# Performance work log

Hardware: AMD Instinct MI355X
Metric: run time of the kernel (lower is better)

The kernel has to match this reference:

```python
import jax, jax.numpy as jnp
import numpy as np

DIM = 128
HEADS = 4
DH = 32
SCALE = DH ** -0.5


def _ln(x, g, b):
    m = x.mean(-1, keepdims=True)
    v = x.var(-1, keepdims=True)
    return (x - m) / jnp.sqrt(v + 1e-5) * g + b


def setup_inputs() -> dict:
    key = jax.random.key(0)
    ks = jax.random.split(key, 16)
    B, N, H, W, HK, WK = 2, 6, 48, 48, 24, 24
    d, hd = DIM, HEADS * DH
    p = lambda k, s: (jax.random.normal(k, s, jnp.float32) * 0.02)
    return {
        "q": jax.random.normal(ks[0], (B, N, d, H, W), jnp.float32),
        "k": jax.random.normal(ks[1], (B, N, d, HK, WK), jnp.float32),
        "v": jax.random.normal(ks[2], (B, N, d, HK, WK), jnp.float32),
        "skip": jax.random.normal(ks[3], (B, d, H, W), jnp.float32),
        "lnq_g": jnp.ones(d), "lnq_b": jnp.zeros(d),
        "Wq": p(ks[4], (d, hd)), "bq": jnp.zeros(hd),
        "lnk_g": jnp.ones(d), "lnk_b": jnp.zeros(d),
        "Wk": p(ks[5], (d, hd)), "bk": jnp.zeros(hd),
        "lnv_g": jnp.ones(d), "lnv_b": jnp.zeros(d),
        "Wv": p(ks[6], (d, hd)), "bv": jnp.zeros(hd),
        "Wp": p(ks[7], (hd, d)), "bp": jnp.zeros(d),
        "pre_g": jnp.ones(d), "pre_b": jnp.zeros(d),
        "W1": p(ks[8], (d, 2 * d)), "b1": jnp.zeros(2 * d),
        "W2": p(ks[9], (2 * d, d)), "b2": jnp.zeros(d),
        "post_g": jnp.ones(d), "post_b": jnp.zeros(d),
    }


def reference(q, k, v, skip, lnq_g, lnq_b, Wq, bq, lnk_g, lnk_b, Wk, bk,
              lnv_g, lnv_b, Wv, bv, Wp, bp, pre_g, pre_b, W1, b1, W2, b2,
              post_g, post_b):
    B, N, d, H, W = q.shape
    _, _, _, HK, WK = k.shape
    Q, K = H * W, HK * WK
    # b n d H W -> b n (H W) d
    qx = q.transpose(0, 1, 3, 4, 2).reshape(B, N, Q, d)
    kx = k.transpose(0, 1, 3, 4, 2).reshape(B, N, K, d)
    vx = v.transpose(0, 1, 3, 4, 2).reshape(B, N * K, d)
    # norm + linear projections
    qp = _ln(qx, lnq_g, lnq_b) @ Wq + bq  # (B,N,Q,HEADS*DH)
    kp = _ln(kx, lnk_g, lnk_b) @ Wk + bk
    vp = _ln(vx, lnv_g, lnv_b) @ Wv + bv  # (B,N*K,HEADS*DH)
    # split heads: b ... (m d) -> (b m) ... d
    qp = qp.reshape(B, N, Q, HEADS, DH).transpose(0, 3, 1, 2, 4).reshape(B * HEADS, N, Q, DH)
    kp = kp.reshape(B, N, K, HEADS, DH).transpose(0, 3, 1, 2, 4).reshape(B * HEADS, N, K, DH)
    vp = vp.reshape(B, N * K, HEADS, DH).transpose(0, 2, 1, 3).reshape(B * HEADS, N * K, DH)
    # per-view scores, then softmax jointly over (n K)
    scores = SCALE * jnp.einsum('bnqd,bnkd->bnqk', qp, kp)
    scores = scores.transpose(0, 2, 1, 3).reshape(B * HEADS, Q, N * K)
    a = jax.nn.softmax(scores, axis=-1)
    out = jnp.einsum('bqk,bkd->bqd', a, vp)  # (B*HEADS, Q, DH)
    # merge heads: (b m) Q d -> b Q (m d)
    z = out.reshape(B, HEADS, Q, DH).transpose(0, 2, 1, 3).reshape(B, Q, HEADS * DH)
    z = z @ Wp + bp
    z = z + skip.transpose(0, 2, 3, 1).reshape(B, Q, d)
    z = _ln(z, pre_g, pre_b)
    z = z + (jax.nn.gelu(z @ W1 + b1, approximate=False) @ W2 + b2)
    z = _ln(z, post_g, post_b)
    return z.reshape(B, H, W, d).transpose(0, 3, 1, 2)
```

## Files before the change

kernel.cpp:

```cpp
#include <hip/hip_runtime.h>
#include <cmath>

#define B_    2
#define N_    6
#define D_    128
#define Q_    2304
#define K_    576
#define NK_   3456
#define HEADS_ 4
#define DH_   32
#define SCALE_ 0.17677669529663687f
#define SCLOG2E_ 0.25504672615621814f

typedef __attribute__((ext_vector_type(8))) short bf16x8;
typedef __attribute__((ext_vector_type(4))) float f32x4;

#if defined(__has_builtin)
#if __has_builtin(__builtin_amdgcn_cvt_pk_bf16_f32)
#define HAS_PK_BF16 1
#endif
#endif

static __device__ __forceinline__ unsigned short f2bf(float f) {
  union { float f; unsigned u; } x; x.f = f;
  unsigned u = x.u + 0x7fffu + ((x.u >> 16) & 1u);
  return (unsigned short)(u >> 16);
}
static __device__ __forceinline__ unsigned pkbf(float a, float b) {
#ifdef HAS_PK_BF16
  typedef __attribute__((ext_vector_type(2))) __bf16 vbf2;
  union { vbf2 v; unsigned u; } cv;
  cv.v = __builtin_amdgcn_cvt_pk_bf16_f32(a, b);
  return cv.u;
#else
  return (unsigned)f2bf(a) | ((unsigned)f2bf(b) << 16);
#endif
}

static __device__ __forceinline__ void pl32sw(unsigned &a, unsigned &b) {
  asm("v_permlane32_swap_b32 %0, %1" : "+v"(a), "+v"(b));
}
static __device__ __forceinline__ void pl16sw(unsigned &a, unsigned &b) {
  asm("v_permlane16_swap_b32 %0, %1" : "+v"(a), "+v"(b));
}

__global__ __launch_bounds__(256) void k_prep_wt(
    const float* __restrict__ Wq, const float* __restrict__ Wk,
    const float* __restrict__ Wv, const float* __restrict__ Wp,
    const float* __restrict__ W1, const float* __restrict__ W2,
    unsigned short* __restrict__ WTq, unsigned short* __restrict__ WTk,
    unsigned short* __restrict__ WTv, unsigned short* __restrict__ WTp,
    unsigned short* __restrict__ WT1, unsigned short* __restrict__ WT2)
{
  __shared__ float tile[32][33];
  const int wb = blockIdx.x, t = threadIdx.x;
  const float* src; unsigned short* dst; int Kd, J, tl;
  if      (wb < 16) { src = Wq; dst = WTq; Kd = 128; J = 128; tl = wb; }
  else if (wb < 32) { src = Wk; dst = WTk; Kd = 128; J = 128; tl = wb - 16; }
  else if (wb < 48) { src = Wv; dst = WTv; Kd = 128; J = 128; tl = wb - 32; }
  else if (wb < 64) { src = Wp; dst = WTp; Kd = 128; J = 128; tl = wb - 48; }
  else if (wb < 96) { src = W1; dst = WT1; Kd = 128; J = 256; tl = wb - 64; }
  else              { src = W2; dst = WT2; Kd = 256; J = 128; tl = wb - 96; }
  const int njt = J >> 5;
  const int tj = tl % njt, tk = tl / njt;
#pragma unroll
  for (int i = 0; i < 4; ++i) {
    int idx = t + 256 * i;
    int r = idx >> 5, c = idx & 31;
    tile[r][c] = src[(size_t)(tk * 32 + r) * J + tj * 32 + c];
  }
  __syncthreads();
#pragma unroll
  for (int i = 0; i < 2; ++i) {
    int idx = t + 256 * i;
    int rr = idx >> 4, c2 = (idx & 15) << 1;
    *(unsigned*)&dst[(size_t)(tj * 32 + rr) * Kd + tk * 32 + c2] =
        pkbf(tile[c2][rr], tile[c2 + 1][rr]);
  }
}

__global__ __launch_bounds__(256) void k_ln_proj_all(
    const float* __restrict__ qin, const float* __restrict__ kin,
    const float* __restrict__ vin,
    const float* __restrict__ lnq_g, const float* __restrict__ lnq_b,
    const float* __restrict__ lnk_g, const float* __restrict__ lnk_b,
    const float* __restrict__ lnv_g, const float* __restrict__ lnv_b,
    const unsigned short* __restrict__ WTq, const unsigned short* __restrict__ WTk,
    const unsigned short* __restrict__ WTv,
    const float* __restrict__ bq, const float* __restrict__ bk,
    const float* __restrict__ bv,
    unsigned short* __restrict__ QPh, unsigned short* __restrict__ KPh,
    unsigned short* __restrict__ VPTh)
{
  __shared__ float xs[32][132];
  __shared__ unsigned short xh[32][136];
  __shared__ float gs[128], bs[128];
  __shared__ float mu[32], rsd[32];
  const int t = threadIdx.x;
  const int bid = blockIdx.x;

  const float* x; const unsigned short* WT; const float* g; const float* bl;
  const float* bias; int S, blk, mode; float osc;
  if (bid < 864)       { mode = 0; blk = bid;        x = qin; WT = WTq; g = lnq_g; bl = lnq_b; bias = bq; S = Q_; osc = SCLOG2E_; }
  else if (bid < 1080) { mode = 0; blk = bid - 864;  x = kin; WT = WTk; g = lnk_g; bl = lnk_b; bias = bk; S = K_; osc = 1.0f; }
  else                 { mode = 1; blk = bid - 1080; x = vin; WT = WTv; g = lnv_g; bl = lnv_b; bias = bv; S = K_; osc = 1.0f; }
  const int ntile = S >> 5;
  const int o  = blk / ntile;
  const int s0 = (blk % ntile) << 5;

  if (t < 128) { gs[t] = g[t]; bs[t] = bl[t]; }
  const float* xb = x + (size_t)o * 128 * (size_t)S + s0;
#pragma unroll
  for (int i = 0; i < 4; ++i) {
    int idx = t + 256 * i;
    int c = idx >> 3, s4 = (idx & 7) << 2;
    float4 xv = *(const float4*)&xb[(size_t)c * S + s4];
    xs[s4 + 0][c] = xv.x; xs[s4 + 1][c] = xv.y;
    xs[s4 + 2][c] = xv.z; xs[s4 + 3][c] = xv.w;
  }
  __syncthreads();
  {
    int s = t >> 3, l8 = t & 7;
    float sum = 0.f, sq = 0.f;
    for (int c = l8; c < 128; c += 8) { float v = xs[s][c]; sum += v; sq += v * v; }
#pragma unroll
    for (int off = 4; off > 0; off >>= 1) {
      sum += __shfl_down(sum, off, 8);
      sq  += __shfl_down(sq,  off, 8);
    }
    if (l8 == 0) {
      float mth = sum * 0.0078125f;
      float var = sq * 0.0078125f - mth * mth;
      mu[s] = mth; rsd[s] = rsqrtf(var + 1e-5f);
    }
  }
  __syncthreads();
#pragma unroll
  for (int i = 0; i < 8; ++i) {
    int idx = t + 256 * i;
    int s = idx >> 6, c2 = (idx & 63) << 1;
    float y0 = (xs[s][c2]     - mu[s]) * rsd[s] * gs[c2]     + bs[c2];
    float y1 = (xs[s][c2 + 1] - mu[s]) * rsd[s] * gs[c2 + 1] + bs[c2 + 1];
    *(unsigned*)&xh[s][c2] = pkbf(y0, y1);
  }
  __syncthreads();
  const int w = t >> 6, lane = t & 63, quad = lane >> 4, l16 = lane & 15;
  const f32x4 zf = {0.f, 0.f, 0.f, 0.f};
  f32x4 acc[2][2] = {{zf, zf}, {zf, zf}};
#pragma unroll
  for (int kc = 0; kc < 4; ++kc) {
    bf16x8 a0 = *(const bf16x8*)&xh[l16][kc * 32 + quad * 8];
    bf16x8 a1 = *(const bf16x8*)&xh[16 + l16][kc * 32 + quad * 8];
    bf16x8 b0 = *(const bf16x8*)&WT[(size_t)(w * 32 + l16) * 128 + kc * 32 + quad * 8];
    bf16x8 b1 = *(const bf16x8*)&WT[(size_t)(w * 32 + 16 + l16) * 128 + kc * 32 + quad * 8];
    acc[0][0] = __builtin_amdgcn_mfma_f32_16x16x32_bf16(a0, b0, acc[0][0], 0, 0, 0);
    acc[0][1] = __builtin_amdgcn_mfma_f32_16x16x32_bf16(a0, b1, acc[0][1], 0, 0, 0);
    acc[1][0] = __builtin_amdgcn_mfma_f32_16x16x32_bf16(a1, b0, acc[1][0], 0, 0, 0);
    acc[1][1] = __builtin_amdgcn_mfma_f32_16x16x32_bf16(a1, b1, acc[1][1], 0, 0, 0);
  }
  if (mode == 0) {
    unsigned short* outh = (bid < 864) ? QPh : KPh;
    __syncthreads();
#pragma unroll
    for (int mt = 0; mt < 2; ++mt)
#pragma unroll
      for (int nt = 0; nt < 2; ++nt) {
        int col = w * 32 + nt * 16 + l16;
        float bc = bias[col];
#pragma unroll
        for (int r = 0; r < 4; ++r)
          xh[mt * 16 + quad * 4 + r][col] = f2bf((acc[mt][nt][r] + bc) * osc);
      }
    __syncthreads();
#pragma unroll
    for (int i = 0; i < 2; ++i) {
      int s = i * 16 + (t >> 4), c8 = (t & 15) << 3;
      *(uint4*)&outh[((size_t)o * S + s0 + s) * 128 + c8] = *(uint4*)&xh[s][c8];
    }
  } else {
    const int b = o / 6, n = o % 6;
#pragma unroll
    for (int mt = 0; mt < 2; ++mt)
#pragma unroll
      for (int nt = 0; nt < 2; ++nt) {
        int col = w * 32 + nt * 16 + l16;
        int hh = col >> 5, dh = col & 31;
        float bc = bias[col];
        ushort4 pk;
        *(unsigned*)&pk.x = pkbf(acc[mt][nt][0] + bc, acc[mt][nt][1] + bc);
        *(unsigned*)&pk.z = pkbf(acc[mt][nt][2] + bc, acc[mt][nt][3] + bc);
        int s = n * 576 + s0 + mt * 16 + quad * 4;
        *(ushort4*)&VPTh[((size_t)(b * 4 + hh) * 32 + dh) * (size_t)NK_ + s] = pk;
      }
  }
}

__global__ __launch_bounds__(256) void k_attn_mfma(
    const unsigned short* __restrict__ QPh, const unsigned short* __restrict__ KPh,
    const unsigned short* __restrict__ VPTh, float* __restrict__ PO,
    float* __restrict__ Pl, int sh)
{
  __shared__ float ol[4][16][32];
  __shared__ float ll[4][2][4][16];
  const int t = threadIdx.x;
  const int w = t >> 6, lane = t & 63;
  const int quad = lane >> 4, l16 = lane & 15;
  const int qt = blockIdx.x % 72;
  const int rest = blockIdx.x / 72;
  const int bhx = rest & 7, ks = rest >> 3;
  const int bb = bhx >> 2, h = bhx & 3;
  const int q0 = qt << 5;

  const unsigned short* vbase = VPTh + (size_t)bhx * 32 * (size_t)NK_;
  const f32x4 zf = {0.f, 0.f, 0.f, 0.f};
  f32x4 o00 = zf, o01 = zf, o10 = zf, o11 = zf;
  float lsum0 = 0.f, lsum1 = 0.f;

  const int m8 = ks * 4 + w;
  int c0 = (108 * m8) >> sh, c1 = (108 * (m8 + 1)) >> sh;

  while (c0 < c1) {
    const int nn = c0 / 18;
    const int cend = min(c1, (nn + 1) * 18);
    const unsigned short* kb = &KPh[((size_t)(bb * 6 + nn) * K_) * 128 + h * 32];
    const unsigned short* qb = &QPh[((size_t)(bb * 6 + nn) * Q_ + q0) * 128 + h * 32];
    bf16x8 qc0 = *(const bf16x8*)&qb[(size_t)l16 * 128 + quad * 8];
    bf16x8 qc1 = *(const bf16x8*)&qb[(size_t)(16 + l16) * 128 + quad * 8];

    int kl = (c0 - nn * 18) << 5;
    bf16x8 kf0 = *(const bf16x8*)&kb[(size_t)(kl + l16) * 128 + quad * 8];
    bf16x8 kf1 = *(const bf16x8*)&kb[(size_t)(kl + 16 + l16) * 128 + quad * 8];
    const unsigned short* vb = vbase + ((size_t)c0 << 5);
    bf16x8 pv0 = *(const bf16x8*)&vb[(size_t)l16 * NK_ + quad * 8];
    bf16x8 pv1 = *(const bf16x8*)&vb[(size_t)(16 + l16) * NK_ + quad * 8];
    f32x4 s00 = __builtin_amdgcn_mfma_f32_16x16x32_bf16(kf0, qc0, zf, 0, 0, 0);
    f32x4 s01 = __builtin_amdgcn_mfma_f32_16x16x32_bf16(kf1, qc0, zf, 0, 0, 0);
    f32x4 s10 = __builtin_amdgcn_mfma_f32_16x16x32_bf16(kf0, qc1, zf, 0, 0, 0);
    f32x4 s11 = __builtin_amdgcn_mfma_f32_16x16x32_bf16(kf1, qc1, zf, 0, 0, 0);

    for (int kc = c0; kc < cend; ++kc) {
      const int kln = (kc + 1 - nn * 18) << 5;
      bf16x8 nk0 = *(const bf16x8*)&kb[(size_t)(kln + l16) * 128 + quad * 8];
      bf16x8 nk1 = *(const bf16x8*)&kb[(size_t)(kln + 16 + l16) * 128 + quad * 8];
      const unsigned short* vbn = vbase + ((size_t)(kc + 1) << 5);
      bf16x8 nv0 = *(const bf16x8*)&vbn[(size_t)l16 * NK_ + quad * 8];
      bf16x8 nv1 = *(const bf16x8*)&vbn[(size_t)(16 + l16) * NK_ + quad * 8];

      float a00 = __builtin_amdgcn_exp2f(s00.x), a01 = __builtin_amdgcn_exp2f(s00.y);
      float a02 = __builtin_amdgcn_exp2f(s00.z), a03 = __builtin_amdgcn_exp2f(s00.w);
      float a10 = __builtin_amdgcn_exp2f(s01.x), a11 = __builtin_amdgcn_exp2f(s01.y);
      float a12 = __builtin_amdgcn_exp2f(s01.z), a13 = __builtin_amdgcn_exp2f(s01.w);
      lsum0 += (a00 + a01 + a02 + a03) + (a10 + a11 + a12 + a13);
      float b00 = __builtin_amdgcn_exp2f(s10.x), b01 = __builtin_amdgcn_exp2f(s10.y);
      float b02 = __builtin_amdgcn_exp2f(s10.z), b03 = __builtin_amdgcn_exp2f(s10.w);
      float b10 = __builtin_amdgcn_exp2f(s11.x), b11 = __builtin_amdgcn_exp2f(s11.y);
      float b12 = __builtin_amdgcn_exp2f(s11.z), b13 = __builtin_amdgcn_exp2f(s11.w);
      lsum1 += (b00 + b01 + b02 + b03) + (b10 + b11 + b12 + b13);

      unsigned xA0 = pkbf(a00, a01), xA1 = pkbf(a02, a03);
      unsigned xB0 = pkbf(a10, a11), xB1 = pkbf(a12, a13);
      unsigned yA0 = pkbf(b00, b01), yA1 = pkbf(b02, b03);
      unsigned yB0 = pkbf(b10, b11), yB1 = pkbf(b12, b13);
      pl32sw(xA0, xB0); pl32sw(xA1, xB1);
      pl16sw(xA0, xB0); pl16sw(xA1, xB1);
      pl32sw(yA0, yB0); pl32sw(yA1, yB1);
      pl16sw(yA0, yB0); pl16sw(yA1, yB1);
      union { unsigned u[4]; bf16x8 v; } f0, f1;
      f0.u[0] = xA0; f0.u[1] = xA1; f0.u[2] = xB0; f0.u[3] = xB1;
      f1.u[0] = yA0; f1.u[1] = yA1; f1.u[2] = yB0; f1.u[3] = yB1;

      __builtin_amdgcn_s_setprio(1);
      o00 = __builtin_amdgcn_mfma_f32_16x16x32_bf16(f0.v, pv0, o00, 0, 0, 0);
      o01 = __builtin_amdgcn_mfma_f32_16x16x32_bf16(f0.v, pv1, o01, 0, 0, 0);
      o10 = __builtin_amdgcn_mfma_f32_16x16x32_bf16(f1.v, pv0, o10, 0, 0, 0);
      o11 = __builtin_amdgcn_mfma_f32_16x16x32_bf16(f1.v, pv1, o11, 0, 0, 0);
      s00 = __builtin_amdgcn_mfma_f32_16x16x32_bf16(nk0, qc0, zf, 0, 0, 0);
      s01 = __builtin_amdgcn_mfma_f32_16x16x32_bf16(nk1, qc0, zf, 0, 0, 0);
      s10 = __builtin_amdgcn_mfma_f32_16x16x32_bf16(nk0, qc1, zf, 0, 0, 0);
      s11 = __builtin_amdgcn_mfma_f32_16x16x32_bf16(nk1, qc1, zf, 0, 0, 0);
      __builtin_amdgcn_s_setprio(0);
      pv0 = nv0; pv1 = nv1;
    }
    c0 = cend;
  }

  ll[w][0][quad][l16] = lsum0;
  ll[w][1][quad][l16] = lsum1;
#pragma unroll
  for (int tt = 0; tt < 2; ++tt) {
    __syncthreads();
    f32x4 t0 = tt ? o10 : o00;
    f32x4 t1 = tt ? o11 : o01;
#pragma unroll
    for (int r = 0; r < 4; ++r) {
      ol[w][quad * 4 + r][l16]      = t0[r];
      ol[w][quad * 4 + r][16 + l16] = t1[r];
    }
    __syncthreads();
    const int q = t >> 4, i16 = t & 15, dd = i16 << 1;
    float a0 = 0.f, a1 = 0.f;
#pragma unroll
    for (int ww = 0; ww < 4; ++ww) { a0 += ol[ww][q][dd]; a1 += ol[ww][q][dd + 1]; }
    float2 r2; r2.x = a0; r2.y = a1;
    *(float2*)&PO[(((size_t)ks * 8 + bhx) * Q_ + q0 + tt * 16 + q) * 32 + dd] = r2;
    if (i16 == 0) {
      float l = 0.f;
#pragma unroll
      for (int ww = 0; ww < 4; ++ww)
#pragma unroll
        for (int qq = 0; qq < 4; ++qq) l += ll[ww][tt][qq][q];
      Pl[((size_t)ks * 8 + bhx) * Q_ + q0 + tt * 16 + q] = l;
    }
  }
}

__global__ __launch_bounds__(512) void k_tail(
    const float* __restrict__ PO, const float* __restrict__ Pl,
    const unsigned short* __restrict__ WTp, const float* __restrict__ bp,
    const float* __restrict__ skip,
    const float* __restrict__ pre_g, const float* __restrict__ pre_b,
    const unsigned short* __restrict__ WT1, const float* __restrict__ b1,
    const unsigned short* __restrict__ WT2, const float* __restrict__ b2,
    const float* __restrict__ post_g, const float* __restrict__ post_b,
    float* __restrict__ out, int nks)
{
  __shared__ float xs[16][132];
  __shared__ unsigned short xh[16][136];
  __shared__ unsigned short hb[16][264];
  __shared__ float g1s[128], b1s[128], g2s[128], b2s[128];
  __shared__ float mu[16], rsd[16];
  const int t = threadIdx.x;
  const int row0 = blockIdx.x << 4;
  const int bb = row0 / Q_, hw0 = row0 % Q_;
  const int w = t >> 6, lane = t & 63, quad = lane >> 4, l16 = lane & 15;
  const f32x4 zf = {0.f, 0.f, 0.f, 0.f};

  if (t < 128) { g1s[t] = pre_g[t]; b1s[t] = pre_b[t]; g2s[t] = post_g[t]; b2s[t] = post_b[t]; }
#pragma unroll
  for (int i = 0; i < 2; ++i) {
    int idx = t + 512 * i;
    int s = idx >> 6, c2 = (idx & 63) << 1;
    int q = hw0 + s;
    int h = c2 >> 5, dh = c2 & 31;
    size_t bq = (size_t)(bb * 4 + h) * Q_ + q;
    size_t i0 = bq * 32 + dh;
    float px = 0.f, py = 0.f, l = 0.f;
    for (int p = 0; p < nks; ++p) {
      float2 pp = *(const float2*)&PO[(size_t)p * 589824 + i0];
      px += pp.x; py += pp.y;
      l += Pl[(size_t)p * 18432 + bq];
    }
    float inv = 1.f / l;
    *(unsigned*)&xh[s][c2] = pkbf(px * inv, py * inv);
  }
  __syncthreads();
  {
    f32x4 acc = zf;
    const int col = w * 16 + l16;
#pragma unroll
    for (int kc = 0; kc < 4; ++kc) {
      bf16x8 a0 = *(const bf16x8*)&xh[l16][kc * 32 + quad * 8];
      bf16x8 b0 = *(const bf16x8*)&WTp[(size_t)col * 128 + kc * 32 + quad * 8];
      acc = __builtin_amdgcn_mfma_f32_16x16x32_bf16(a0, b0, acc, 0, 0, 0);
    }
    float bc = bp[col];
    float4 sk = *(const float4*)&skip[((size_t)bb * 128 + col) * Q_ + hw0 + quad * 4];
    xs[quad * 4 + 0][col] = acc[0] + bc + sk.x;
    xs[quad * 4 + 1][col] = acc[1] + bc + sk.y;
    xs[quad * 4 + 2][col] = acc[2] + bc + sk.z;
    xs[quad * 4 + 3][col] = acc[3] + bc + sk.w;
  }
  __syncthreads();
  {
    int s = t >> 5, lg = t & 31;
    float sum = 0.f, sq = 0.f;
    for (int c = lg; c < 128; c += 32) { float v = xs[s][c]; sum += v; sq += v * v; }
#pragma unroll
    for (int off = 16; off > 0; off >>= 1) {
      sum += __shfl_down(sum, off, 32);
      sq  += __shfl_down(sq,  off, 32);
    }
    if (lg == 0) {
      float mth = sum * 0.0078125f;
      float var = sq * 0.0078125f - mth * mth;
      mu[s] = mth; rsd[s] = rsqrtf(var + 1e-5f);
    }
  }
  __syncthreads();
#pragma unroll
  for (int i = 0; i < 2; ++i) {
    int idx = t + 512 * i;
    int s = idx >> 6, c2 = (idx & 63) << 1;
    float y0 = (xs[s][c2]     - mu[s]) * rsd[s] * g1s[c2]     + b1s[c2];
    float y1 = (xs[s][c2 + 1] - mu[s]) * rsd[s] * g1s[c2 + 1] + b1s[c2 + 1];
    xs[s][c2] = y0; xs[s][c2 + 1] = y1;
    *(unsigned*)&xh[s][c2] = pkbf(y0, y1);
  }
  __syncthreads();
  {
#pragma unroll
    for (int nt = 0; nt < 2; ++nt) {
      const int col = w * 32 + nt * 16 + l16;
      f32x4 acc = zf;
#pragma unroll
      for (int kc = 0; kc < 4; ++kc) {
        bf16x8 a0 = *(const bf16x8*)&xh[l16][kc * 32 + quad * 8];
        bf16x8 b0 = *(const bf16x8*)&WT1[(size_t)col * 128 + kc * 32 + quad * 8];
        acc = __builtin_amdgcn_mfma_f32_16x16x32_bf16(a0, b0, acc, 0, 0, 0);
      }
      float bc = b1[col];
#pragma unroll
      for (int r = 0; r < 4; ++r) {
        float hx = acc[r] + bc;
        hb[quad * 4 + r][col] =
            f2bf(0.5f * hx * (1.f + erff(hx * 0.7071067811865476f)));
      }
    }
  }
  __syncthreads();
  {
    f32x4 acc = zf;
    const int col = w * 16 + l16;
#pragma unroll
    for (int kc = 0; kc < 8; ++kc) {
      bf16x8 a0 = *(const bf16x8*)&hb[l16][kc * 32 + quad * 8];
      bf16x8 b0 = *(const bf16x8*)&WT2[(size_t)col * 256 + kc * 32 + quad * 8];
      acc = __builtin_amdgcn_mfma_f32_16x16x32_bf16(a0, b0, acc, 0, 0, 0);
    }
    float bc = b2[col];
#pragma unroll
    for (int r = 0; r < 4; ++r) {
      int row = quad * 4 + r;
      xs[row][col] = acc[r] + bc + xs[row][col];
    }
  }
  __syncthreads();
  {
    int s = t >> 5, lg = t & 31;
    float sum = 0.f, sq = 0.f;
    for (int c = lg; c < 128; c += 32) { float v = xs[s][c]; sum += v; sq += v * v; }
#pragma unroll
    for (int off = 16; off > 0; off >>= 1) {
      sum += __shfl_down(sum, off, 32);
      sq  += __shfl_down(sq,  off, 32);
    }
    if (lg == 0) {
      float mth = sum * 0.0078125f;
      float var = sq * 0.0078125f - mth * mth;
      mu[s] = mth; rsd[s] = rsqrtf(var + 1e-5f);
    }
  }
  __syncthreads();
#pragma unroll
  for (int i = 0; i < 4; ++i) {
    int idx = t + 512 * i;
    int s = idx & 15, c = idx >> 4;
    out[(size_t)bb * (128 * (size_t)Q_) + (size_t)c * Q_ + hw0 + s] =
        (xs[s][c] - mu[s]) * rsd[s] * g2s[c] + b2s[c];
  }
}

extern "C" void kernel_launch(void* const* d_in, const int* in_sizes, int n_in,
                              void* d_out, int out_size, void* d_ws, size_t ws_size,
                              hipStream_t stream) {
  const float* q     = (const float*)d_in[0];
  const float* k     = (const float*)d_in[1];
  const float* v     = (const float*)d_in[2];
  const float* skip  = (const float*)d_in[3];
  const float* lnq_g = (const float*)d_in[4];
  const float* lnq_b = (const float*)d_in[5];
  const float* Wq    = (const float*)d_in[6];
  const float* bq    = (const float*)d_in[7];
  const float* lnk_g = (const float*)d_in[8];
  const float* lnk_b = (const float*)d_in[9];
  const float* Wk    = (const float*)d_in[10];
  const float* bk    = (const float*)d_in[11];
  const float* lnv_g = (const float*)d_in[12];
  const float* lnv_b = (const float*)d_in[13];
  const float* Wv    = (const float*)d_in[14];
  const float* bvv   = (const float*)d_in[15];
  const float* Wp    = (const float*)d_in[16];
  const float* bp    = (const float*)d_in[17];
  const float* pre_g = (const float*)d_in[18];
  const float* pre_b = (const float*)d_in[19];
  const float* W1    = (const float*)d_in[20];
  const float* b1    = (const float*)d_in[21];
  const float* W2    = (const float*)d_in[22];
  const float* b2    = (const float*)d_in[23];
  const float* post_g= (const float*)d_in[24];
  const float* post_b= (const float*)d_in[25];
  float* out = (float*)d_out;

  int nks = 2, sh = 3;
  if (ws_size >= (size_t)20611072) { nks = 4; sh = 4; }
  unsigned short* QPh  = (unsigned short*)d_ws;
  unsigned short* KPh  = QPh + 3538944;
  unsigned short* VPTh = KPh + 884736;
  float* PO  = (float*)(VPTh + 884736);
  float* Pl  = PO + (size_t)nks * 589824;
  unsigned short* WTq = (unsigned short*)(Pl + (size_t)nks * 18432);
  unsigned short* WTk = WTq + 16384;
  unsigned short* WTv = WTk + 16384;
  unsigned short* WTp = WTv + 16384;
  unsigned short* WT1 = WTp + 16384;
  unsigned short* WT2 = WT1 + 32768;

  k_prep_wt<<<dim3(128), dim3(256), 0, stream>>>(Wq, Wk, Wv, Wp, W1, W2,
                                                 WTq, WTk, WTv, WTp, WT1, WT2);
  k_ln_proj_all<<<dim3(1296), dim3(256), 0, stream>>>(
      q, k, v, lnq_g, lnq_b, lnk_g, lnk_b, lnv_g, lnv_b,
      WTq, WTk, WTv, bq, bk, bvv, QPh, KPh, VPTh);
  k_attn_mfma<<<dim3(72 * 8 * nks), dim3(256), 0, stream>>>(QPh, KPh, VPTh, PO, Pl, sh);
  k_tail<<<dim3(288), dim3(512), 0, stream>>>(PO, Pl, WTp, bp, skip,
                                              pre_g, pre_b, WT1, b1, WT2, b2,
                                              post_g, post_b, out, nks);
}
```

Baseline: 178.8 us.

## Split attention by view, share K/V tiles via LDS, reduce partials with atomics

The attention kernel is restructured so each block handles one view and four 32-query tiles, one per wave. The block cooperatively stages each K and V chunk into double-buffered, swizzled shared memory so the four waves share one copy, replacing per-wave global loads. Partial outputs and softmax denominators are accumulated with float atomics into a single buffer that the weight-prep kernel now zeroes. The LDS cross-wave reduction and multi-slice partial buffers go away, at the cost of a block barrier per chunk and heavy atomic traffic (six views per output).

```diff
diff --git a/kernel.cpp b/kernel.cpp
--- a/kernel.cpp
+++ b/kernel.cpp
@@ -50,10 +50,16 @@
     const float* __restrict__ W1, const float* __restrict__ W2,
     unsigned short* __restrict__ WTq, unsigned short* __restrict__ WTk,
     unsigned short* __restrict__ WTv, unsigned short* __restrict__ WTp,
-    unsigned short* __restrict__ WT1, unsigned short* __restrict__ WT2)
+    unsigned short* __restrict__ WT1, unsigned short* __restrict__ WT2,
+    float* __restrict__ Z, int zn)
 {
   __shared__ float tile[32][33];
   const int wb = blockIdx.x, t = threadIdx.x;
+  {
+    const float4 z4 = {0.f, 0.f, 0.f, 0.f};
+    for (int i = wb * 256 + t; i < zn; i += 128 * 256)
+      ((float4*)Z)[i] = z4;
+  }
   const float* src; unsigned short* dst; int Kd, J, tl;
   if      (wb < 16) { src = Wq; dst = WTq; Kd = 128; J = 128; tl = wb; }
   else if (wb < 32) { src = Wk; dst = WTk; Kd = 128; J = 128; tl = wb - 16; }
@@ -198,119 +204,106 @@
 __global__ __launch_bounds__(256) void k_attn_mfma(
     const unsigned short* __restrict__ QPh, const unsigned short* __restrict__ KPh,
     const unsigned short* __restrict__ VPTh, float* __restrict__ PO,
-    float* __restrict__ Pl, int sh)
+    float* __restrict__ Pl)
 {
-  __shared__ float ol[4][16][32];
-  __shared__ float ll[4][2][4][16];
+  __shared__ __align__(16) unsigned short smem[2][2048];
   const int t = threadIdx.x;
   const int w = t >> 6, lane = t & 63;
   const int quad = lane >> 4, l16 = lane & 15;
-  const int qt = blockIdx.x % 72;
-  const int rest = blockIdx.x / 72;
-  const int bhx = rest & 7, ks = rest >> 3;
+  const int qg  = blockIdx.x % 18;
+  const int rest = blockIdx.x / 18;
+  const int bhx = rest & 7, nn = rest >> 3;
   const int bb = bhx >> 2, h = bhx & 3;
-  const int q0 = qt << 5;
-
-  const unsigned short* vbase = VPTh + (size_t)bhx * 32 * (size_t)NK_;
+  const int q0 = (qg * 4 + w) << 5;
+
+  const unsigned short* kb = KPh + ((size_t)(bb * 6 + nn) * K_) * 128 + h * 32;
+  const unsigned short* qb = QPh + ((size_t)(bb * 6 + nn) * Q_ + q0) * 128 + h * 32;
+  const unsigned short* vb = VPTh + (size_t)bhx * 32 * (size_t)NK_ + (size_t)nn * 18 * 32;
+
+  bf16x8 qc0 = *(const bf16x8*)&qb[(size_t)l16 * 128 + quad * 8];
+  bf16x8 qc1 = *(const bf16x8*)&qb[(size_t)(16 + l16) * 128 + quad * 8];
+
+  const int row16 = l16 + ((w & 1) << 4);
+  const int xsl = (quad ^ ((l16 >> 1) & 3)) << 3;
+  const unsigned short* sbase = (w < 2)
+      ? kb + (size_t)row16 * 128 + quad * 8
+      : vb + (size_t)row16 * NK_ + quad * 8;
+  const int sstride = (w < 2) ? 4096 : 32;
+  const int wdst = ((w >= 2) ? 1024 : 0) + row16 * 32 + xsl;
+
   const f32x4 zf = {0.f, 0.f, 0.f, 0.f};
   f32x4 o00 = zf, o01 = zf, o10 = zf, o11 = zf;
   float lsum0 = 0.f, lsum1 = 0.f;
 
-  const int m8 = ks * 4 + w;
-  int c0 = (108 * m8) >> sh, c1 = (108 * (m8 + 1)) >> sh;
-
-  while (c0 < c1) {
-    const int nn = c0 / 18;
-    const int cend = min(c1, (nn + 1) * 18);
-    const unsigned short* kb = &KPh[((size_t)(bb * 6 + nn) * K_) * 128 + h * 32];
-    const unsigned short* qb = &QPh[((size_t)(bb * 6 + nn) * Q_ + q0) * 128 + h * 32];
-    bf16x8 qc0 = *(const bf16x8*)&qb[(size_t)l16 * 128 + quad * 8];
-    bf16x8 qc1 = *(const bf16x8*)&qb[(size_t)(16 + l16) * 128 + quad * 8];
-
-    int kl = (c0 - nn * 18) << 5;
-    bf16x8 kf0 = *(const bf16x8*)&kb[(size_t)(kl + l16) * 128 + quad * 8];
-    bf16x8 kf1 = *(const bf16x8*)&kb[(size_t)(kl + 16 + l16) * 128 + quad * 8];
-    const unsigned short* vb = vbase + ((size_t)c0 << 5);
-    bf16x8 pv0 = *(const bf16x8*)&vb[(size_t)l16 * NK_ + quad * 8];
-    bf16x8 pv1 = *(const bf16x8*)&vb[(size_t)(16 + l16) * NK_ + quad * 8];
+  uint4 st0 = *(const uint4*)&sbase[0];
+  uint4 stn = *(const uint4*)&sbase[sstride];
+  *(uint4*)&smem[0][wdst] = st0;
+  __syncthreads();
+
+#pragma unroll 2
+  for (int kc = 0; kc < 18; ++kc) {
+    const int buf = kc & 1;
+    if (kc < 17) *(uint4*)&smem[buf ^ 1][wdst] = stn;
+    if (kc < 16) stn = *(const uint4*)&sbase[(size_t)(kc + 2) * sstride];
+
+    const unsigned short* sb = &smem[buf][0];
+    bf16x8 kf0 = *(const bf16x8*)&sb[l16 * 32 + xsl];
+    bf16x8 kf1 = *(const bf16x8*)&sb[(16 + l16) * 32 + xsl];
+    bf16x8 pv0 = *(const bf16x8*)&sb[1024 + l16 * 32 + xsl];
+    bf16x8 pv1 = *(const bf16x8*)&sb[1024 + (16 + l16) * 32 + xsl];
+
+    __builtin_amdgcn_s_setprio(1);
     f32x4 s00 = __builtin_amdgcn_mfma_f32_16x16x32_bf16(kf0, qc0, zf, 0, 0, 0);
     f32x4 s01 = __builtin_amdgcn_mfma_f32_16x16x32_bf16(kf1, qc0, zf, 0, 0, 0);
     f32x4 s10 = __builtin_amdgcn_mfma_f32_16x16x32_bf16(kf0, qc1, zf, 0, 0, 0);
     f32x4 s11 = __builtin_amdgcn_mfma_f32_16x16x32_bf16(kf1, qc1, zf, 0, 0, 0);
 
-    for (int kc = c0; kc < cend; ++kc) {
-      const int kln = (kc + 1 - nn * 18) << 5;
-      bf16x8 nk0 = *(const bf16x8*)&kb[(size_t)(kln + l16) * 128 + quad * 8];
-      bf16x8 nk1 = *(const bf16x8*)&kb[(size_t)(kln + 16 + l16) * 128 + quad * 8];
-      const unsigned short* vbn = vbase + ((size_t)(kc + 1) << 5);
-      bf16x8 nv0 = *(const bf16x8*)&vbn[(size_t)l16 * NK_ + quad * 8];
-      bf16x8 nv1 = *(const bf16x8*)&vbn[(size_t)(16 + l16) * NK_ + quad * 8];
-
-      float a00 = __builtin_amdgcn_exp2f(s00.x), a01 = __builtin_amdgcn_exp2f(s00.y);
-      float a02 = __builtin_amdgcn_exp2f(s00.z), a03 = __builtin_amdgcn_exp2f(s00.w);
-      float a10 = __builtin_amdgcn_exp2f(s01.x), a11 = __builtin_amdgcn_exp2f(s01.y);
-      float a12 = __builtin_amdgcn_exp2f(s01.z), a13 = __builtin_amdgcn_exp2f(s01.w);
-      lsum0 += (a00 + a01 + a02 + a03) + (a10 + a11 + a12 + a13);
-      float b00 = __builtin_amdgcn_exp2f(s10.x), b01 = __builtin_amdgcn_exp2f(s10.y);
-      float b02 = __builtin_amdgcn_exp2f(s10.z), b03 = __builtin_amdgcn_exp2f(s10.w);
-      float b10 = __builtin_amdgcn_exp2f(s11.x), b11 = __builtin_amdgcn_exp2f(s11.y);
-      float b12 = __builtin_amdgcn_exp2f(s11.z), b13 = __builtin_amdgcn_exp2f(s11.w);
-      lsum1 += (b00 + b01 + b02 + b03) + (b10 + b11 + b12 + b13);
-
-      unsigned xA0 = pkbf(a00, a01), xA1 = pkbf(a02, a03);
-      unsigned xB0 = pkbf(a10, a11), xB1 = pkbf(a12, a13);
-      unsigned yA0 = pkbf(b00, b01), yA1 = pkbf(b02, b03);
-      unsigned yB0 = pkbf(b10, b11), yB1 = pkbf(b12, b13);
-      pl32sw(xA0, xB0); pl32sw(xA1, xB1);
-      pl16sw(xA0, xB0); pl16sw(xA1, xB1);
-      pl32sw(yA0, yB0); pl32sw(yA1, yB1);
-      pl16sw(yA0, yB0); pl16sw(yA1, yB1);
-      union { unsigned u[4]; bf16x8 v; } f0, f1;
-      f0.u[0] = xA0; f0.u[1] = xA1; f0.u[2] = xB0; f0.u[3] = xB1;
-      f1.u[0] = yA0; f1.u[1] = yA1; f1.u[2] = yB0; f1.u[3] = yB1;
-
-      __builtin_amdgcn_s_setprio(1);
-      o00 = __builtin_amdgcn_mfma_f32_16x16x32_bf16(f0.v, pv0, o00, 0, 0, 0);
-      o01 = __builtin_amdgcn_mfma_f32_16x16x32_bf16(f0.v, pv1, o01, 0, 0, 0);
-      o10 = __builtin_amdgcn_mfma_f32_16x16x32_bf16(f1.v, pv0, o10, 0, 0, 0);
-      o11 = __builtin_amdgcn_mfma_f32_16x16x32_bf16(f1.v, pv1, o11, 0, 0, 0);
-      s00 = __builtin_amdgcn_mfma_f32_16x16x32_bf16(nk0, qc0, zf, 0, 0, 0);
-      s01 = __builtin_amdgcn_mfma_f32_16x16x32_bf16(nk1, qc0, zf, 0, 0, 0);
-      s10 = __builtin_amdgcn_mfma_f32_16x16x32_bf16(nk0, qc1, zf, 0, 0, 0);
-      s11 = __builtin_amdgcn_mfma_f32_16x16x32_bf16(nk1, qc1, zf, 0, 0, 0);
-      __builtin_amdgcn_s_setprio(0);
-      pv0 = nv0; pv1 = nv1;
-    }
-    c0 = cend;
-  }
-
-  ll[w][0][quad][l16] = lsum0;
-  ll[w][1][quad][l16] = lsum1;
-#pragma unroll
-  for (int tt = 0; tt < 2; ++tt) {
+    float a00 = __builtin_amdgcn_exp2f(s00.x), a01 = __builtin_amdgcn_exp2f(s00.y);
+    float a02 = __builtin_amdgcn_exp2f(s00.z), a03 = __builtin_amdgcn_exp2f(s00.w);
+    float a10 = __builtin_amdgcn_exp2f(s01.x), a11 = __builtin_amdgcn_exp2f(s01.y);
+    float a12 = __builtin_amdgcn_exp2f(s01.z), a13 = __builtin_amdgcn_exp2f(s01.w);
+    lsum0 += (a00 + a01 + a02 + a03) + (a10 + a11 + a12 + a13);
+    float b00 = __builtin_amdgcn_exp2f(s10.x), b01 = __builtin_amdgcn_exp2f(s10.y);
+    float b02 = __builtin_amdgcn_exp2f(s10.z), b03 = __builtin_amdgcn_exp2f(s10.w);
+    float b10 = __builtin_amdgcn_exp2f(s11.x), b11 = __builtin_amdgcn_exp2f(s11.y);
+    float b12 = __builtin_amdgcn_exp2f(s11.z), b13 = __builtin_amdgcn_exp2f(s11.w);
+    lsum1 += (b00 + b01 + b02 + b03) + (b10 + b11 + b12 + b13);
+
+    unsigned xA0 = pkbf(a00, a01), xA1 = pkbf(a02, a03);
+    unsigned xB0 = pkbf(a10, a11), xB1 = pkbf(a12, a13);
+    unsigned yA0 = pkbf(b00, b01), yA1 = pkbf(b02, b03);
+    unsigned yB0 = pkbf(b10, b11), yB1 = pkbf(b12, b13);
+    pl32sw(xA0, xB0); pl32sw(xA1, xB1);
+    pl16sw(xA0, xB0); pl16sw(xA1, xB1);
+    pl32sw(yA0, yB0); pl32sw(yA1, yB1);
+    pl16sw(yA0, yB0); pl16sw(yA1, yB1);
+    union { unsigned u[4]; bf16x8 v; } f0, f1;
+    f0.u[0] = xA0; f0.u[1] = xA1; f0.u[2] = xB0; f0.u[3] = xB1;
+    f1.u[0] = yA0; f1.u[1] = yA1; f1.u[2] = yB0; f1.u[3] = yB1;
+
+    o00 = __builtin_amdgcn_mfma_f32_16x16x32_bf16(f0.v, pv0, o00, 0, 0, 0);
+    o01 = __builtin_amdgcn_mfma_f32_16x16x32_bf16(f0.v, pv1, o01, 0, 0, 0);
+    o10 = __builtin_amdgcn_mfma_f32_16x16x32_bf16(f1.v, pv0, o10, 0, 0, 0);
+    o11 = __builtin_amdgcn_mfma_f32_16x16x32_bf16(f1.v, pv1, o11, 0, 0, 0);
+    __builtin_amdgcn_s_setprio(0);
     __syncthreads();
-    f32x4 t0 = tt ? o10 : o00;
-    f32x4 t1 = tt ? o11 : o01;
-#pragma unroll
-    for (int r = 0; r < 4; ++r) {
-      ol[w][quad * 4 + r][l16]      = t0[r];
-      ol[w][quad * 4 + r][16 + l16] = t1[r];
-    }
-    __syncthreads();
-    const int q = t >> 4, i16 = t & 15, dd = i16 << 1;
-    float a0 = 0.f, a1 = 0.f;
-#pragma unroll
-    for (int ww = 0; ww < 4; ++ww) { a0 += ol[ww][q][dd]; a1 += ol[ww][q][dd + 1]; }
-    float2 r2; r2.x = a0; r2.y = a1;
-    *(float2*)&PO[(((size_t)ks * 8 + bhx) * Q_ + q0 + tt * 16 + q) * 32 + dd] = r2;
-    if (i16 == 0) {
-      float l = 0.f;
-#pragma unroll
-      for (int ww = 0; ww < 4; ++ww)
-#pragma unroll
-        for (int qq = 0; qq < 4; ++qq) l += ll[ww][tt][qq][q];
-      Pl[((size_t)ks * 8 + bhx) * Q_ + q0 + tt * 16 + q] = l;
-    }
+  }
+
+  lsum0 += __shfl_xor(lsum0, 16);
+  lsum0 += __shfl_xor(lsum0, 32);
+  lsum1 += __shfl_xor(lsum1, 16);
+  lsum1 += __shfl_xor(lsum1, 32);
+  if (lane < 16) {
+    atomicAdd(&Pl[(size_t)bhx * Q_ + q0 + lane], lsum0);
+    atomicAdd(&Pl[(size_t)bhx * Q_ + q0 + 16 + lane], lsum1);
+  }
+  float* pob = PO + ((size_t)bhx * Q_ + q0) * 32;
+#pragma unroll
+  for (int r = 0; r < 4; ++r) {
+    atomicAdd(&pob[(quad * 4 + r) * 32 + l16],           o00[r]);
+    atomicAdd(&pob[(quad * 4 + r) * 32 + 16 + l16],      o01[r]);
+    atomicAdd(&pob[(16 + quad * 4 + r) * 32 + l16],      o10[r]);
+    atomicAdd(&pob[(16 + quad * 4 + r) * 32 + 16 + l16], o11[r]);
   }
 }
 
@@ -322,7 +315,7 @@
     const unsigned short* __restrict__ WT1, const float* __restrict__ b1,
     const unsigned short* __restrict__ WT2, const float* __restrict__ b2,
     const float* __restrict__ post_g, const float* __restrict__ post_b,
-    float* __restrict__ out, int nks)
+    float* __restrict__ out)
 {
   __shared__ float xs[16][132];
   __shared__ unsigned short xh[16][136];
@@ -344,14 +337,9 @@
     int h = c2 >> 5, dh = c2 & 31;
     size_t bq = (size_t)(bb * 4 + h) * Q_ + q;
     size_t i0 = bq * 32 + dh;
-    float px = 0.f, py = 0.f, l = 0.f;
-    for (int p = 0; p < nks; ++p) {
-      float2 pp = *(const float2*)&PO[(size_t)p * 589824 + i0];
-      px += pp.x; py += pp.y;
-      l += Pl[(size_t)p * 18432 + bq];
-    }
-    float inv = 1.f / l;
-    *(unsigned*)&xh[s][c2] = pkbf(px * inv, py * inv);
+    float2 pp = *(const float2*)&PO[i0];
+    float inv = 1.f / Pl[bq];
+    *(unsigned*)&xh[s][c2] = pkbf(pp.x * inv, pp.y * inv);
   }
   __syncthreads();
   {
@@ -491,27 +479,27 @@
   const float* post_b= (const float*)d_in[25];
   float* out = (float*)d_out;
 
-  int nks = 2, sh = 3;
-  if (ws_size >= (size_t)20611072) { nks = 4; sh = 4; }
   unsigned short* QPh  = (unsigned short*)d_ws;
   unsigned short* KPh  = QPh + 3538944;
   unsigned short* VPTh = KPh + 884736;
   float* PO  = (float*)(VPTh + 884736);
-  float* Pl  = PO + (size_t)nks * 589824;
-  unsigned short* WTq = (unsigned short*)(Pl + (size_t)nks * 18432);
+  float* Pl  = PO + 589824;
+  unsigned short* WTq = (unsigned short*)(Pl + 18432);
   unsigned short* WTk = WTq + 16384;
   unsigned short* WTv = WTk + 16384;
   unsigned short* WTp = WTv + 16384;
   unsigned short* WT1 = WTp + 16384;
   unsigned short* WT2 = WT1 + 32768;
+  const int zn = (589824 + 18432) / 4;
 
   k_prep_wt<<<dim3(128), dim3(256), 0, stream>>>(Wq, Wk, Wv, Wp, W1, W2,
-                                                 WTq, WTk, WTv, WTp, WT1, WT2);
+                                                 WTq, WTk, WTv, WTp, WT1, WT2,
+                                                 PO, zn);
   k_ln_proj_all<<<dim3(1296), dim3(256), 0, stream>>>(
       q, k, v, lnq_g, lnq_b, lnk_g, lnk_b, lnv_g, lnv_b,
       WTq, WTk, WTv, bq, bk, bvv, QPh, KPh, VPTh);
-  k_attn_mfma<<<dim3(72 * 8 * nks), dim3(256), 0, stream>>>(QPh, KPh, VPTh, PO, Pl, sh);
+  k_attn_mfma<<<dim3(18 * 8 * 6), dim3(256), 0, stream>>>(QPh, KPh, VPTh, PO, Pl);
   k_tail<<<dim3(288), dim3(512), 0, stream>>>(PO, Pl, WTp, bp, skip,
                                               pre_g, pre_b, WT1, b1, WT2, b2,
-                                              post_g, post_b, out, nks);
-}
+                                              post_g, post_b, out);
+}
```

New measurement: 165.0 us (median of 2 runs). 7.7% less time.
